# Kernel optimization log

Measured on AMD Instinct MI355X. Metric: run time of the kernel, lower is better.

The kernel has to match this reference:

```python
import jax, jax.numpy as jnp
import numpy as np

K = 7          # kernel_size
PAD = ((K - 1) * (1 - 1) + K) // 2  # = 3, 'same' padding for dilation=1


def setup_inputs() -> dict:
    key = jax.random.key(0)
    k1, k2 = jax.random.split(key)
    x = jax.random.normal(k1, (16, 96, 128, 128), dtype=jnp.float32)
    weight = jax.random.normal(k2, (96, K, K), dtype=jnp.float32) * 0.1
    return {"x": x, "weight": weight}


def reference(x, weight):
    """Morphological dilation2d with soft_max=True (ReLU after).

    Equivalent to torch: unfold(x, K, padding=PAD) -> max over window of
    (patch + w). nn.Unfold zero-pads, so borders see literal zeros in the max;
    we reproduce that with jnp.pad (zeros), not -inf padding.
    """
    B, C, H, W = x.shape
    xp = jnp.pad(x, ((0, 0), (0, 0), (PAD, PAD), (PAD, PAD)))  # zero pad, matches nn.Unfold
    out = jnp.full((B, C, H, W), -jnp.inf, dtype=x.dtype)
    # Fixed K*K loop over kernel taps (structural, not data-dim loop):
    # running max avoids materializing the (B,H*W,C,K*K) im2col tensor.
    for i in range(K):
        for j in range(K):
            shifted = jax.lax.dynamic_slice(xp, (0, 0, i, j), (B, C, H, W))
            out = jnp.maximum(out, shifted + weight[None, :, i, j, None, None])
    return jax.nn.relu(out)  # soft_max=True -> ReLU activation
```

## Files before the change

kernel.cpp:

```cpp
#include <hip/hip_runtime.h>

#define HH 128
#define WW 128
#define CC 96
#define KK 7

#define LROWS 70
#define LF (LROWS * WW)
#define NSLOT ((67 * WW) / 4)


typedef __attribute__((address_space(1))) const void gv_t;
typedef __attribute__((address_space(3))) void lv_t;

__device__ __forceinline__ void gload_lds16(const float* g, float* l) {
  __builtin_amdgcn_global_load_lds((gv_t*)g, (lv_t*)(unsigned)(uintptr_t)l,
                                   16, 0, 0);
}

__global__ __launch_bounds__(256, 4) void morph_kernel(
    const float* __restrict__ x, const float* __restrict__ weight,
    float* __restrict__ out) {
  __shared__ float lds[LF];

  const int t = threadIdx.x;
  const int half = blockIdx.x & 1;
  const int plane = blockIdx.x >> 1;
  const int c = plane % CC;

  const float* __restrict__ xp = x + (size_t)plane * (HH * WW);
  float* __restrict__ op = out + (size_t)plane * (HH * WW);
  const float* __restrict__ Wc = weight + c * (KK * KK);

  float wv[KK * KK];
#pragma unroll
  for (int k = 0; k < KK * KK; ++k)
    wv[k] = __int_as_float(__builtin_amdgcn_readfirstlane(__float_as_int(Wc[k])));

  const int rv0 = half ? 0 : 3;
  const int zrow0 = half ? 67 : 0;
  const int grow0 = half ? 61 : 0;

  if (t < 96) {
    *(float4*)&lds[zrow0 * WW + t * 4] = make_float4(0.f, 0.f, 0.f, 0.f);
  }

  {
    const float* gsrc = xp + grow0 * WW;
    float* ldst = &lds[rv0 * WW];
#pragma unroll
    for (int k = 0; k < 9; ++k) {
      const int slot = k * 256 + t;
      if (slot < NSLOT) gload_lds16(gsrc + slot * 4, ldst + slot * 4);
    }
  }
  __syncthreads();

  const int cg = t & 31;
  const int rg = t >> 5;
  const int tc0 = cg << 2;
  const int r0l = rg << 3;
  const bool lok = (tc0 >= 4);
  const bool rok = (tc0 <= WW - 8);

  const float* lp = &lds[r0l * WW + tc0];
  const float* qA = lok ? lp - 4 : lp;
  const float* qB = lp;
  const float* qC = rok ? lp + 4 : lp;

  float acc[8][4];
#pragma unroll
  for (int y = 0; y < 8; ++y)
#pragma unroll
    for (int q = 0; q < 4; ++q) acc[y][q] = 0.f;

  float4 S[2][3];
#define LOAD_STRIP(slot, s)                      \
  do {                                           \
    S[slot][0] = *(const float4*)(qA + (s) * WW); \
    S[slot][1] = *(const float4*)(qB + (s) * WW); \
    S[slot][2] = *(const float4*)(qC + (s) * WW); \
  } while (0)

  LOAD_STRIP(0, 0);

#pragma unroll
  for (int s = 0; s < 14; ++s) {
    if (s + 1 < 14) LOAD_STRIP((s + 1) & 1, s + 1);

    const int sl = s & 1;
    const float4 A = S[sl][0], B = S[sl][1], C = S[sl][2];
    const float e[10] = {lok ? A.y : 0.f, lok ? A.z : 0.f, lok ? A.w : 0.f,
                         B.x, B.y, B.z, B.w,
                         rok ? C.x : 0.f, rok ? C.y : 0.f, rok ? C.z : 0.f};

#pragma unroll
    for (int yl = 0; yl < 8; ++yl) {
      const int i = s - yl;
      if (i < 0 || i >= KK) continue;
      const float w0 = wv[i * 7 + 0], w1 = wv[i * 7 + 1], w2 = wv[i * 7 + 2],
                  w3 = wv[i * 7 + 3], w4 = wv[i * 7 + 4], w5 = wv[i * 7 + 5],
                  w6 = wv[i * 7 + 6];
#pragma unroll
      for (int q = 0; q < 4; ++q) {
        const float t0 = e[q + 0] + w0;
        const float t1 = e[q + 1] + w1;
        const float t2 = e[q + 2] + w2;
        const float t3 = e[q + 3] + w3;
        const float t4 = e[q + 4] + w4;
        const float t5 = e[q + 5] + w5;
        const float t6 = e[q + 6] + w6;
        float m = acc[yl][q];
        m = fmaxf(fmaxf(m, t0), t1);
        m = fmaxf(fmaxf(m, t2), t3);
        m = fmaxf(fmaxf(m, t4), t5);
        acc[yl][q] = fmaxf(m, t6);
      }
    }

    if (s >= 6) {
      const int yl = s - 6;
      float4 o = make_float4(acc[yl][0], acc[yl][1], acc[yl][2], acc[yl][3]);
      *(float4*)(op + (size_t)(half * 64 + r0l + yl) * WW + tc0) = o;
    }
  }
#undef LOAD_STRIP
}

extern "C" void kernel_launch(void* const* d_in, const int* in_sizes, int n_in,
                              void* d_out, int out_size, void* d_ws, size_t ws_size,
                              hipStream_t stream) {
  const float* x = (const float*)d_in[0];
  const float* w = (const float*)d_in[1];
  float* out = (float*)d_out;
  const int nblocks = 16 * CC * 2;
  morph_kernel<<<nblocks, 256, 0, stream>>>(x, w, out);
}
```

Measured before the change: 184.6 us.

## Process whole plane per block with double-buffered LDS row strips

Each block now handles a full 128x128 plane in four 32-row strips instead of a half-plane in one shot. While one strip is being computed, the next strip is loaded asynchronously into a second LDS buffer, so global loads overlap with compute. Out-of-range rows read from a shared zero row. This halves the grid and the per-thread output rows, which lowers occupancy-level parallelism and adds barriers and more halo reloads per strip.

```diff
diff --git a/kernel.cpp b/kernel.cpp
--- a/kernel.cpp
+++ b/kernel.cpp
@@ -5,9 +5,10 @@
 #define CC 96
 #define KK 7
 
-#define LROWS 70
-#define LF (LROWS * WW)
-#define NSLOT ((67 * WW) / 4)
+#define SROWS 38
+#define BUF_F (SROWS * WW)
+#define ZOFS_F (2 * BUF_F)
+#define LDS_F (ZOFS_F + WW)
 
 
 typedef __attribute__((address_space(1))) const void gv_t;
@@ -21,13 +22,13 @@
 __global__ __launch_bounds__(256, 4) void morph_kernel(
     const float* __restrict__ x, const float* __restrict__ weight,
     float* __restrict__ out) {
-  __shared__ float lds[LF];
+  __shared__ float lds[LDS_F];
+  const int t = threadIdx.x;
+  const int wid = t >> 5;
+  const int lid = t & 31;
 
-  const int t = threadIdx.x;
-  const int half = blockIdx.x & 1;
-  const int plane = blockIdx.x >> 1;
+  const int plane = blockIdx.x;
   const int c = plane % CC;
-
   const float* __restrict__ xp = x + (size_t)plane * (HH * WW);
   float* __restrict__ op = out + (size_t)plane * (HH * WW);
   const float* __restrict__ Wc = weight + c * (KK * KK);
@@ -37,94 +38,111 @@
   for (int k = 0; k < KK * KK; ++k)
     wv[k] = __int_as_float(__builtin_amdgcn_readfirstlane(__float_as_int(Wc[k])));
 
-  const int rv0 = half ? 0 : 3;
-  const int zrow0 = half ? 67 : 0;
-  const int grow0 = half ? 61 : 0;
+  float* const buf0 = &lds[0];
+  float* const buf1 = &lds[BUF_F];
+  float* const zp = &lds[ZOFS_F];
 
-  if (t < 96) {
-    *(float4*)&lds[zrow0 * WW + t * 4] = make_float4(0.f, 0.f, 0.f, 0.f);
-  }
+  if (t < 32) *(float4*)(zp + t * 4) = make_float4(0.f, 0.f, 0.f, 0.f);
 
-  {
-    const float* gsrc = xp + grow0 * WW;
-    float* ldst = &lds[rv0 * WW];
-#pragma unroll
-    for (int k = 0; k < 9; ++k) {
-      const int slot = k * 256 + t;
-      if (slot < NSLOT) gload_lds16(gsrc + slot * 4, ldst + slot * 4);
-    }
-  }
+#define STAGE(qq, lb)                                                        \
+  do {                                                                       \
+    _Pragma("unroll")                                                        \
+    for (int kk = 0; kk < 5; ++kk) {                                         \
+      int row_ = kk * 8 + wid;                                    \
+      int srow_ = (row_ > 37) ? row_ - 2 : row_;                             \
+      int grow_ = (qq) * 32 - 3 + srow_;                                     \
+      grow_ = grow_ < 0 ? 0 : (grow_ > HH - 1 ? HH - 1 : grow_);             \
+      gload_lds16(xp + grow_ * WW + lid * 4, (lb) + srow_ * WW + lid * 4);   \
+    }                                                                        \
+  } while (0)
+
+  STAGE(0, buf0);
   __syncthreads();
 
-  const int cg = t & 31;
-  const int rg = t >> 5;
-  const int tc0 = cg << 2;
-  const int r0l = rg << 3;
+  const int tc0 = lid << 2;
+  const int r0l = wid << 2;
   const bool lok = (tc0 >= 4);
   const bool rok = (tc0 <= WW - 8);
 
-  const float* lp = &lds[r0l * WW + tc0];
-  const float* qA = lok ? lp - 4 : lp;
-  const float* qB = lp;
-  const float* qC = rok ? lp + 4 : lp;
+  for (int k = 0; k < 4; ++k) {
+    float* const cur = (k & 1) ? buf1 : buf0;
+    float* const nxt = (k & 1) ? buf0 : buf1;
 
-  float acc[8][4];
+    if (k < 3) {
+      STAGE(k + 1, nxt);
+      asm volatile("s_waitcnt vmcnt(5)" ::: "memory");
+    } else {
+      asm volatile("s_waitcnt vmcnt(0)" ::: "memory");
+    }
+    __builtin_amdgcn_sched_barrier(0);
+    __builtin_amdgcn_s_barrier();
+
+    float acc[4][4];
 #pragma unroll
-  for (int y = 0; y < 8; ++y)
+    for (int y = 0; y < 4; ++y)
 #pragma unroll
-    for (int q = 0; q < 4; ++q) acc[y][q] = 0.f;
+      for (int q = 0; q < 4; ++q) acc[y][q] = 0.f;
 
-  float4 S[2][3];
-#define LOAD_STRIP(slot, s)                      \
-  do {                                           \
-    S[slot][0] = *(const float4*)(qA + (s) * WW); \
-    S[slot][1] = *(const float4*)(qB + (s) * WW); \
-    S[slot][2] = *(const float4*)(qC + (s) * WW); \
-  } while (0)
+    const float* vb = cur + r0l * WW + tc0;
+    const int gq0 = k * 32 - 3 + r0l;
 
-  LOAD_STRIP(0, 0);
+    float4 S[2][3];
+#define LOAD_STRIP(slot, s)                                                  \
+    do {                                                                     \
+      const bool rv_ = (unsigned)(gq0 + (s)) < (unsigned)HH;                 \
+      const float* bs_ = rv_ ? (vb + (s) * WW) : zp;                         \
+      const float* pA_ = (rv_ && lok) ? bs_ - 4 : zp;                        \
+      const float* pC_ = (rv_ && rok) ? bs_ + 4 : zp;                        \
+      S[slot][0] = *(const float4*)pA_;                                      \
+      S[slot][1] = *(const float4*)bs_;                                      \
+      S[slot][2] = *(const float4*)pC_;                                      \
+    } while (0)
+
+    LOAD_STRIP(0, 0);
+#pragma unroll
+    for (int s = 0; s < 10; ++s) {
+      if (s + 1 < 10) LOAD_STRIP((s + 1) & 1, s + 1);
+      const int sl = s & 1;
+      const float4 A = S[sl][0], B = S[sl][1], C = S[sl][2];
+      const float e[10] = {A.y, A.z, A.w, B.x, B.y, B.z, B.w, C.x, C.y, C.z};
 
 #pragma unroll
-  for (int s = 0; s < 14; ++s) {
-    if (s + 1 < 14) LOAD_STRIP((s + 1) & 1, s + 1);
+      for (int yl = 0; yl < 4; ++yl) {
+        const int i = s - yl;
+        if (i < 0 || i >= KK) continue;
+        const float w0 = wv[i * 7 + 0], w1 = wv[i * 7 + 1], w2 = wv[i * 7 + 2],
+                    w3 = wv[i * 7 + 3], w4 = wv[i * 7 + 4], w5 = wv[i * 7 + 5],
+                    w6 = wv[i * 7 + 6];
+#pragma unroll
+        for (int q = 0; q < 4; ++q) {
+          const float t0 = e[q + 0] + w0;
+          const float t1 = e[q + 1] + w1;
+          const float t2 = e[q + 2] + w2;
+          const float t3 = e[q + 3] + w3;
+          const float t4 = e[q + 4] + w4;
+          const float t5 = e[q + 5] + w5;
+          const float t6 = e[q + 6] + w6;
+          float m = acc[yl][q];
+          m = fmaxf(fmaxf(m, t0), t1);
+          m = fmaxf(fmaxf(m, t2), t3);
+          m = fmaxf(fmaxf(m, t4), t5);
+          acc[yl][q] = fmaxf(m, t6);
+        }
+      }
 
-    const int sl = s & 1;
-    const float4 A = S[sl][0], B = S[sl][1], C = S[sl][2];
-    const float e[10] = {lok ? A.y : 0.f, lok ? A.z : 0.f, lok ? A.w : 0.f,
-                         B.x, B.y, B.z, B.w,
-                         rok ? C.x : 0.f, rok ? C.y : 0.f, rok ? C.z : 0.f};
-
-#pragma unroll
-    for (int yl = 0; yl < 8; ++yl) {
-      const int i = s - yl;
-      if (i < 0 || i >= KK) continue;
-      const float w0 = wv[i * 7 + 0], w1 = wv[i * 7 + 1], w2 = wv[i * 7 + 2],
-                  w3 = wv[i * 7 + 3], w4 = wv[i * 7 + 4], w5 = wv[i * 7 + 5],
-                  w6 = wv[i * 7 + 6];
-#pragma unroll
-      for (int q = 0; q < 4; ++q) {
-        const float t0 = e[q + 0] + w0;
-        const float t1 = e[q + 1] + w1;
-        const float t2 = e[q + 2] + w2;
-        const float t3 = e[q + 3] + w3;
-        const float t4 = e[q + 4] + w4;
-        const float t5 = e[q + 5] + w5;
-        const float t6 = e[q + 6] + w6;
-        float m = acc[yl][q];
-        m = fmaxf(fmaxf(m, t0), t1);
-        m = fmaxf(fmaxf(m, t2), t3);
-        m = fmaxf(fmaxf(m, t4), t5);
-        acc[yl][q] = fmaxf(m, t6);
+      if (s >= 6) {
+        const int yl = s - 6;
+        *(float4*)(op + (size_t)(k * 32 + r0l + yl) * WW + tc0) =
+            make_float4(acc[yl][0], acc[yl][1], acc[yl][2], acc[yl][3]);
       }
     }
+#undef LOAD_STRIP
 
-    if (s >= 6) {
-      const int yl = s - 6;
-      float4 o = make_float4(acc[yl][0], acc[yl][1], acc[yl][2], acc[yl][3]);
-      *(float4*)(op + (size_t)(half * 64 + r0l + yl) * WW + tc0) = o;
-    }
+    asm volatile("s_waitcnt lgkmcnt(0)" ::: "memory");
+    __builtin_amdgcn_s_barrier();
+    __builtin_amdgcn_sched_barrier(0);
   }
-#undef LOAD_STRIP
+#undef STAGE
 }
 
 extern "C" void kernel_launch(void* const* d_in, const int* in_sizes, int n_in,
@@ -133,6 +151,6 @@
   const float* x = (const float*)d_in[0];
   const float* w = (const float*)d_in[1];
   float* out = (float*)d_out;
-  const int nblocks = 16 * CC * 2;
+  const int nblocks = 16 * CC;
   morph_kernel<<<nblocks, 256, 0, stream>>>(x, w, out);
 }
```

After: 188.8 us. +2.3%, slower.
